# Performance work log

Measured on AMD Instinct MI355X. Metric: run time of the kernel, lower is better.

The kernel has to match this reference:

```python
import jax, jax.numpy as jnp
import numpy as np
import math

N = 30000; N0 = 18000; N1 = 12000; R = 5; E = 600000
H = 128; HM = 128; C = 8
L1 = 20.0; L2 = 30.0
THRESH = 0.3; THRESH_C = 1e-3
T_INNER = 20; K_OUTER = 8
EPS = 1e-5


def setup_inputs() -> dict:
    key = jax.random.key(0)
    ks = jax.random.split(key, 16)
    def w(k, shape):  # kaiming-ish fan_in init
        return jax.random.normal(k, shape, jnp.float32) / np.sqrt(shape[0])
    return {
        "feat0": jax.random.normal(ks[0], (N0, 256), jnp.float32),
        "feat1": jax.random.normal(ks[1], (N1, 128), jnp.float32),
        "W0": w(ks[2], (256, H)), "b0": jnp.zeros((H,), jnp.float32),
        "W1": w(ks[3], (128, H)), "b1": jnp.zeros((H,), jnp.float32),
        "Wm1": w(ks[4], (H, HM)), "bm1": jnp.zeros((HM,), jnp.float32),
        "Wm2": w(ks[5], (HM, HM)), "bm2": jnp.zeros((HM,), jnp.float32),
        "Wout": w(ks[6], (HM, C)), "bout": jnp.zeros((C,), jnp.float32),
        "src": jax.random.randint(ks[7], (E,), 0, N, jnp.int32),
        "dst": jax.random.randint(ks[8], (E,), 0, N, jnp.int32),
        "rel": jax.random.randint(ks[9], (E,), 0, R, jnp.int32),
    }


def _layernorm(z):
    m = z.mean(-1, keepdims=True)
    v = z.var(-1, keepdims=True)
    return (z - m) / jnp.sqrt(v + EPS)


def _forward(feat0, feat1, W0, b0, W1, b1, Wm1, bm1, Wm2, bm2, Wout, bout, src, dst, rel):
    # transfer (transf_type==2): per-type linear -> concat -> 2-layer MLP w/ layernorm
    h = jnp.concatenate([feat0 @ W0 + b0, feat1 @ W1 + b1], axis=0)   # (N, H)
    z = jax.nn.relu(_layernorm(h @ Wm1 + bm1))
    h = z @ Wm2 + bm2                                                 # (N, HM)
    # per-node standardization (torch std is unbiased, ddof=1), nan -> 0
    mu = h.mean(1, keepdims=True)
    sd = h.std(1, ddof=1, keepdims=True)
    out0 = jnp.nan_to_num((h - mu) / sd)

    # per-relation row degrees of the vertically stacked adjacency (R*N, N)
    key_e = rel * N + src                                             # (E,)
    deg = jax.ops.segment_sum(jnp.ones(E, jnp.float32), key_e, num_segments=R * N)
    safe = jnp.maximum(deg, 1.0)
    vals = jnp.where(deg > 0, 1.0 / safe, 0.0)[key_e]                 # row-normalized A weights
    dinv = jnp.where(deg > 0, 1.0 / jnp.sqrt(safe), 0.0)              # D^{-1/2}
    edge_dinv = dinv[key_e] * dinv[rel * N + dst]                     # (E,)
    active = (deg > 0).astype(jnp.float32).reshape(R, N)              # (R, N)

    def tv(x):  # relational total variation tr(X^T L_r X)/N, L_r = I - D^-1/2 A_r D^-1/2
        node_term = active @ (x * x).sum(1)                           # (R,)
        edot = (x[src] * x[dst]).sum(1)                               # (E,)
        edge_term = jax.ops.segment_sum(edge_dinv * edot, rel, num_segments=R)
        return (node_term - edge_term) / N

    ratio = 2.0 * L2 / L1
    c_l1tr = jnp.abs(tv(out0)).sum()
    u0 = jnp.full((R,), 1.0 / R, jnp.float32)

    def mirror_descent(u, w, l1tr):
        fi = l1tr + ratio
        def step(carry, t):
            u, act = carry
            T_t = jnp.sqrt(2.0 * math.log(R) / (t * fi * fi))
            u_ta = u * jnp.exp(-T_t * (ratio * u + w))
            u_new = u_ta / u_ta.sum()
            diff = jnp.sqrt(((u - u_new) ** 2).sum())
            u = jnp.where(act, u_new, u)
            return (u, act & (diff >= THRESH_C)), None
        ts = jnp.arange(1, T_INNER + 1, dtype=jnp.float32)
        (u, _), _ = jax.lax.scan(step, (u, jnp.array(True)), ts)
        return u

    def outer(carry, _):
        x, u, act = carry
        w = tv(x)
        l1tr = jnp.abs(w).sum()
        u = jnp.where(act, mirror_descent(u, w, l1tr), u)
        still = act & (l1tr / c_l1tr >= THRESH)
        ew = u[rel] * vals                                            # (E,)
        msg = jax.ops.segment_sum(ew[:, None] * x[dst], src, num_segments=N)  # (N, HM)
        x = jnp.where(still, x / (1.0 + L1) + (L1 / (1.0 + L1)) * msg, x)
        return (x, u, still), None

    (x, u, _), _ = jax.lax.scan(outer, (out0, u0, jnp.array(True)), None, length=K_OUTER)
    logits = x @ Wout + bout
    return logits, x, u


def reference(feat0, feat1, W0, b0, W1, b1, Wm1, bm1, Wm2, bm2, Wout, bout, src, dst, rel):
    return _forward(feat0, feat1, W0, b0, W1, b1, Wm1, bm1, Wm2, bm2, Wout, bout, src, dst, rel)
```

## Files before the change

### kernel.cpp

```cpp
#include <hip/hip_runtime.h>
#include <cmath>

typedef unsigned short ushort_t;
typedef unsigned int uint_t;

#define N_TOT 30000
#define N0_   18000
#define R_    5
#define E_    600000
#define RN    (R_ * N_TOT)
#define NC_   (N_TOT * 8)
#define NX_   (N_TOT * 128)
#define SCAN_NB ((RN + 1023) / 1024)

typedef __attribute__((ext_vector_type(8))) short bf16x8;
typedef __attribute__((ext_vector_type(4))) float f32x4;

__device__ __forceinline__ ushort_t f2bf(float f) {
    uint_t u = __float_as_uint(f);
    uint_t r = (u + 0x7fffu + ((u >> 16) & 1u)) >> 16;
    return (ushort_t)r;
}
__device__ __forceinline__ float bflo(uint_t v) { return __uint_as_float(v << 16); }
__device__ __forceinline__ float bfhi(uint_t v) { return __uint_as_float(v & 0xffff0000u); }

__global__ void init_kernel(float* ug, int* act) {
    if (threadIdx.x < 5) ug[threadIdx.x] = 0.2f;
    if (threadIdx.x == 0) act[0] = 1;
}

__global__ __launch_bounds__(256) void cvtfeat_kernel(const float* __restrict__ in,
                                                      ushort_t* __restrict__ out,
                                                      int nelem)
{
    int i = (blockIdx.x * 256 + threadIdx.x) * 4;
    if (i >= nelem) return;
    const float4 v = *(const float4*)(in + i);
    ushort_t o0 = f2bf(v.x), o1 = f2bf(v.y), o2 = f2bf(v.z), o3 = f2bf(v.w);
    uint_t p0 = (uint_t)o0 | ((uint_t)o1 << 16);
    uint_t p1 = (uint_t)o2 | ((uint_t)o3 << 16);
    uint2* op = (uint2*)(out + i);
    *op = make_uint2(p0, p1);
}

__global__ __launch_bounds__(256) void cvtw_kernel(const float* __restrict__ W,
                                                   ushort_t* __restrict__ wt, int K)
{
    int idx = blockIdx.x * 256 + threadIdx.x;
    if (idx >= 128 * K) return;
    int j = idx / K, k = idx - j * K;
    wt[idx] = f2bf(W[k * 128 + j]);
}

__global__ __launch_bounds__(256) void mlp_mfma_kernel(
    const ushort_t* __restrict__ fb0, const ushort_t* __restrict__ fb1,
    const ushort_t* __restrict__ wt0, const ushort_t* __restrict__ wt1,
    const ushort_t* __restrict__ wtm1, const ushort_t* __restrict__ wtm2,
    const float* __restrict__ b0, const float* __restrict__ b1,
    const float* __restrict__ bm1, const float* __restrict__ bm2,
    float* __restrict__ xout, ushort_t* __restrict__ xh)
{
    const int t = threadIdx.x;
    const int lane = t & 63;
    const int wv = t >> 6;
    const int lr = lane & 15;
    const int lg = lane >> 4;
    const int row0 = blockIdx.x * 32;

    __shared__ ushort_t hls[32][136];
    __shared__ float    tls[32][132];
    __shared__ ushort_t zls[32][136];

    #pragma unroll
    for (int mt = 0; mt < 2; ++mt) {
        const int rb = row0 + mt * 16;
        const bool is0 = (rb < N0_);
        const int r = min(rb + lr, N_TOT - 1);
        const ushort_t* __restrict__ fa =
            is0 ? fb0 + (size_t)r * 256 : fb1 + (size_t)(r - N0_) * 128;
        const ushort_t* __restrict__ wt = is0 ? wt0 : wt1;
        const int K = is0 ? 256 : 128;
        const int c0 = wv * 32 + lr;

        f32x4 a0 = {0.f, 0.f, 0.f, 0.f};
        f32x4 a1 = {0.f, 0.f, 0.f, 0.f};
        for (int ks = 0; ks < K; ks += 32) {
            const bf16x8 af = *(const bf16x8*)(fa + ks + lg * 8);
            const bf16x8 wb0 = *(const bf16x8*)(wt + (size_t)c0 * K + ks + lg * 8);
            const bf16x8 wb1 = *(const bf16x8*)(wt + (size_t)(c0 + 16) * K + ks + lg * 8);
            a0 = __builtin_amdgcn_mfma_f32_16x16x32_bf16(af, wb0, a0, 0, 0, 0);
            a1 = __builtin_amdgcn_mfma_f32_16x16x32_bf16(af, wb1, a1, 0, 0, 0);
        }
        const float bb0 = is0 ? b0[c0] : b1[c0];
        const float bb1 = is0 ? b0[c0 + 16] : b1[c0 + 16];
        #pragma unroll
        for (int j = 0; j < 4; ++j) {
            hls[mt * 16 + lg * 4 + j][c0]      = f2bf(a0[j] + bb0);
            hls[mt * 16 + lg * 4 + j][c0 + 16] = f2bf(a1[j] + bb1);
        }
    }
    __syncthreads();

    {
        const int c0 = wv * 32 + lr;
        f32x4 g00 = {0.f,0.f,0.f,0.f}, g01 = {0.f,0.f,0.f,0.f};
        f32x4 g10 = {0.f,0.f,0.f,0.f}, g11 = {0.f,0.f,0.f,0.f};
        for (int ks = 0; ks < 128; ks += 32) {
            const bf16x8 wb0 = *(const bf16x8*)(wtm1 + (size_t)c0 * 128 + ks + lg * 8);
            const bf16x8 wb1 = *(const bf16x8*)(wtm1 + (size_t)(c0 + 16) * 128 + ks + lg * 8);
            const bf16x8 af0 = *(const bf16x8*)(&hls[lr][ks + lg * 8]);
            const bf16x8 af1 = *(const bf16x8*)(&hls[16 + lr][ks + lg * 8]);
            g00 = __builtin_amdgcn_mfma_f32_16x16x32_bf16(af0, wb0, g00, 0, 0, 0);
            g01 = __builtin_amdgcn_mfma_f32_16x16x32_bf16(af0, wb1, g01, 0, 0, 0);
            g10 = __builtin_amdgcn_mfma_f32_16x16x32_bf16(af1, wb0, g10, 0, 0, 0);
            g11 = __builtin_amdgcn_mfma_f32_16x16x32_bf16(af1, wb1, g11, 0, 0, 0);
        }
        const float bb0 = bm1[c0], bb1 = bm1[c0 + 16];
        #pragma unroll
        for (int j = 0; j < 4; ++j) {
            tls[lg * 4 + j][c0]           = g00[j] + bb0;
            tls[lg * 4 + j][c0 + 16]      = g01[j] + bb1;
            tls[16 + lg * 4 + j][c0]      = g10[j] + bb0;
            tls[16 + lg * 4 + j][c0 + 16] = g11[j] + bb1;
        }
    }
    __syncthreads();

    {
        const int row = t >> 3, seg = t & 7;
        f32x4 v[4];
        float s = 0.f;
        #pragma unroll
        for (int i = 0; i < 4; ++i) {
            v[i] = *(const f32x4*)(&tls[row][seg * 16 + i * 4]);
            s += v[i][0] + v[i][1] + v[i][2] + v[i][3];
        }
        #pragma unroll
        for (int o = 1; o < 8; o <<= 1) s += __shfl_xor(s, o, 64);
        const float mean = s * (1.0f / 128.0f);
        float q = 0.f;
        #pragma unroll
        for (int i = 0; i < 4; ++i) {
            #pragma unroll
            for (int e = 0; e < 4; ++e) { float d = v[i][e] - mean; q = fmaf(d, d, q); }
        }
        #pragma unroll
        for (int o = 1; o < 8; o <<= 1) q += __shfl_xor(q, o, 64);
        const float inv = 1.0f / sqrtf(q * (1.0f / 128.0f) + 1e-5f);
        uint_t* zp = (uint_t*)&zls[row][0];
        #pragma unroll
        for (int i = 0; i < 4; ++i) {
            ushort_t z0 = f2bf(fmaxf((v[i][0] - mean) * inv, 0.0f));
            ushort_t z1 = f2bf(fmaxf((v[i][1] - mean) * inv, 0.0f));
            ushort_t z2 = f2bf(fmaxf((v[i][2] - mean) * inv, 0.0f));
            ushort_t z3 = f2bf(fmaxf((v[i][3] - mean) * inv, 0.0f));
            zp[(seg * 16 + i * 4) / 2]     = (uint_t)z0 | ((uint_t)z1 << 16);
            zp[(seg * 16 + i * 4) / 2 + 1] = (uint_t)z2 | ((uint_t)z3 << 16);
        }
    }
    __syncthreads();

    {
        const int c0 = wv * 32 + lr;
        f32x4 g00 = {0.f,0.f,0.f,0.f}, g01 = {0.f,0.f,0.f,0.f};
        f32x4 g10 = {0.f,0.f,0.f,0.f}, g11 = {0.f,0.f,0.f,0.f};
        for (int ks = 0; ks < 128; ks += 32) {
            const bf16x8 wb0 = *(const bf16x8*)(wtm2 + (size_t)c0 * 128 + ks + lg * 8);
            const bf16x8 wb1 = *(const bf16x8*)(wtm2 + (size_t)(c0 + 16) * 128 + ks + lg * 8);
            const bf16x8 af0 = *(const bf16x8*)(&zls[lr][ks + lg * 8]);
            const bf16x8 af1 = *(const bf16x8*)(&zls[16 + lr][ks + lg * 8]);
            g00 = __builtin_amdgcn_mfma_f32_16x16x32_bf16(af0, wb0, g00, 0, 0, 0);
            g01 = __builtin_amdgcn_mfma_f32_16x16x32_bf16(af0, wb1, g01, 0, 0, 0);
            g10 = __builtin_amdgcn_mfma_f32_16x16x32_bf16(af1, wb0, g10, 0, 0, 0);
            g11 = __builtin_amdgcn_mfma_f32_16x16x32_bf16(af1, wb1, g11, 0, 0, 0);
        }
        __syncthreads();
        const float bb0 = bm2[c0], bb1 = bm2[c0 + 16];
        #pragma unroll
        for (int j = 0; j < 4; ++j) {
            tls[lg * 4 + j][c0]           = g00[j] + bb0;
            tls[lg * 4 + j][c0 + 16]      = g01[j] + bb1;
            tls[16 + lg * 4 + j][c0]      = g10[j] + bb0;
            tls[16 + lg * 4 + j][c0 + 16] = g11[j] + bb1;
        }
    }
    __syncthreads();

    {
        const int row = t >> 3, seg = t & 7;
        const int n = row0 + row;
        f32x4 v[4];
        float s = 0.f;
        #pragma unroll
        for (int i = 0; i < 4; ++i) {
            v[i] = *(const f32x4*)(&tls[row][seg * 16 + i * 4]);
            s += v[i][0] + v[i][1] + v[i][2] + v[i][3];
        }
        #pragma unroll
        for (int o = 1; o < 8; o <<= 1) s += __shfl_xor(s, o, 64);
        const float mu = s * (1.0f / 128.0f);
        float q = 0.f;
        #pragma unroll
        for (int i = 0; i < 4; ++i) {
            #pragma unroll
            for (int e = 0; e < 4; ++e) { float d = v[i][e] - mu; q = fmaf(d, d, q); }
        }
        #pragma unroll
        for (int o = 1; o < 8; o <<= 1) q += __shfl_xor(q, o, 64);
        const float sd = sqrtf(q * (1.0f / 127.0f));
        const float inv = 1.0f / sd;
        if (n < N_TOT) {
            uint_t* xhp = (uint_t*)xh + (size_t)n * 64 + seg * 8;
            float* xop = xout + (size_t)n * 128 + seg * 16;
            #pragma unroll
            for (int i = 0; i < 4; ++i) {
                float rr[4];
                #pragma unroll
                for (int e = 0; e < 4; ++e) {
                    float r = (v[i][e] - mu) * inv;
                    if (!(fabsf(r) <= 3.402823466e38f)) {
                        r = (r != r) ? 0.0f : ((r > 0.0f) ? 3.402823466e38f : -3.402823466e38f);
                    }
                    rr[e] = r;
                }
                *(float4*)(xop + i * 4) = make_float4(rr[0], rr[1], rr[2], rr[3]);
                xhp[i * 2]     = (uint_t)f2bf(rr[0]) | ((uint_t)f2bf(rr[1]) << 16);
                xhp[i * 2 + 1] = (uint_t)f2bf(rr[2]) | ((uint_t)f2bf(rr[3]) << 16);
            }
        }
    }
}

__global__ void deg_kernel(const int* __restrict__ src, const int* __restrict__ rel,
                           int* __restrict__ deg_i)
{
    int e = blockIdx.x * 256 + threadIdx.x;
    if (e >= E_) return;
    atomicAdd(&deg_i[src[e] * R_ + rel[e]], 1);
}

__global__ void dinv_kernel(const int* __restrict__ deg_i, float* __restrict__ dinv)
{
    int i = blockIdx.x * 256 + threadIdx.x;
    if (i >= RN) return;
    int dg = deg_i[i];
    dinv[i] = (dg > 0) ? 1.0f / sqrtf((float)dg) : 0.0f;
}

__global__ __launch_bounds__(256) void scan1_kernel(const int* __restrict__ cnt,
                                                    int* __restrict__ rp,
                                                    int* __restrict__ bsum)
{
    __shared__ int wsum[4];
    const int t = threadIdx.x, lane = t & 63, w = t >> 6;
    const int i0 = blockIdx.x * 1024 + t * 4;
    const int v0 = (i0 + 0 < RN) ? cnt[i0 + 0] : 0;
    const int v1 = (i0 + 1 < RN) ? cnt[i0 + 1] : 0;
    const int v2 = (i0 + 2 < RN) ? cnt[i0 + 2] : 0;
    const int v3 = (i0 + 3 < RN) ? cnt[i0 + 3] : 0;
    const int s = v0 + v1 + v2 + v3;
    int sc = s;
    #pragma unroll
    for (int o = 1; o < 64; o <<= 1) { int tmp = __shfl_up(sc, o, 64); if (lane >= o) sc += tmp; }
    if (lane == 63) wsum[w] = sc;
    __syncthreads();
    int woff = 0;
    #pragma unroll
    for (int i = 0; i < 3; ++i) if (i < w) woff += wsum[i];
    int run = woff + sc - s;
    if (i0 + 0 < RN) rp[i0 + 0] = run; run += v0;
    if (i0 + 1 < RN) rp[i0 + 1] = run; run += v1;
    if (i0 + 2 < RN) rp[i0 + 2] = run; run += v2;
    if (i0 + 3 < RN) rp[i0 + 3] = run;
    if (t == 255) bsum[blockIdx.x] = woff + sc;
}

__global__ __launch_bounds__(256) void scan2_kernel(const int* __restrict__ bsum,
                                                    int* __restrict__ boff,
                                                    int* __restrict__ rp)
{
    __shared__ int wsum[4];
    const int t = threadIdx.x, lane = t & 63, w = t >> 6;
    const int v = (t < SCAN_NB) ? bsum[t] : 0;
    int sc = v;
    #pragma unroll
    for (int o = 1; o < 64; o <<= 1) { int tmp = __shfl_up(sc, o, 64); if (lane >= o) sc += tmp; }
    if (lane == 63) wsum[w] = sc;
    __syncthreads();
    int woff = 0;
    #pragma unroll
    for (int i = 0; i < 3; ++i) if (i < w) woff += wsum[i];
    boff[t] = woff + sc - v;
    if (t == 0) rp[RN] = E_;
}

__global__ __launch_bounds__(256) void scan3_kernel(int* __restrict__ rp,
                                                    const int* __restrict__ boff)
{
    const int off = boff[blockIdx.x];
    if (off == 0) return;
    const int i0 = blockIdx.x * 1024 + threadIdx.x * 4;
    if (i0 + 3 < RN) {
        int4* p = (int4*)(rp + i0);
        int4 q = *p;
        q.x += off; q.y += off; q.z += off; q.w += off;
        *p = q;
    } else {
        for (int i = 0; i < 4; ++i)
            if (i0 + i < RN) rp[i0 + i] += off;
    }
}

__global__ void scatter_kernel(const int* __restrict__ src, const int* __restrict__ dst,
                               const int* __restrict__ rel, const int* __restrict__ rp,
                               int* __restrict__ fill, const int* __restrict__ deg_i,
                               const float* __restrict__ dinv,
                               int* __restrict__ csr_dst, float* __restrict__ csr_w,
                               float* __restrict__ csr_edinv)
{
    int e = blockIdx.x * 256 + threadIdx.x;
    if (e >= E_) return;
    int s = src[e], r = rel[e], d = dst[e];
    int key = s * R_ + r;
    int pos = rp[key] + atomicAdd(&fill[key], 1);
    csr_dst[pos] = d;
    csr_w[pos] = 1.0f / (float)deg_i[key];
    csr_edinv[pos] = dinv[key] * dinv[d * R_ + r];
}

__global__ __launch_bounds__(256) void tv_kernel(
    const ushort_t* __restrict__ xh, const int* __restrict__ rp,
    const int* __restrict__ csr_dst, const float* __restrict__ csr_edinv,
    const int* __restrict__ act, int k, float* __restrict__ accbuf)
{
    if (act[k] == 0) return;
    const int lane = threadIdx.x & 63;
    const int wv = threadIdx.x >> 6;
    const int wid = blockIdx.x * 4 + wv;
    const int nw = gridDim.x * 4;
    float na[5] = {0, 0, 0, 0, 0};
    float ea[5] = {0, 0, 0, 0, 0};
    for (int n = wid; n < N_TOT; n += nw) {
        const int b0 = __builtin_amdgcn_readfirstlane(rp[n * R_ + 0]);
        const int b1 = __builtin_amdgcn_readfirstlane(rp[n * R_ + 1]);
        const int b2 = __builtin_amdgcn_readfirstlane(rp[n * R_ + 2]);
        const int b3 = __builtin_amdgcn_readfirstlane(rp[n * R_ + 3]);
        const int b4 = __builtin_amdgcn_readfirstlane(rp[n * R_ + 4]);
        const int b5 = __builtin_amdgcn_readfirstlane(rp[n * R_ + 5]);
        const uint_t vs = ((const uint_t*)(xh + (size_t)n * 128))[lane];
        const float sx = bflo(vs), sy = bfhi(vs);
        const float pp = fmaf(sx, sx, sy * sy);
        if (b1 > b0) na[0] += pp;
        if (b2 > b1) na[1] += pp;
        if (b3 > b2) na[2] += pp;
        if (b4 > b3) na[3] += pp;
        if (b5 > b4) na[4] += pp;
        int e = b0;
        for (; e + 4 <= b5; e += 4) {
            const int dn0 = csr_dst[e + 0];
            const int dn1 = csr_dst[e + 1];
            const int dn2 = csr_dst[e + 2];
            const int dn3 = csr_dst[e + 3];
            const float w0 = csr_edinv[e + 0];
            const float w1 = csr_edinv[e + 1];
            const float w2 = csr_edinv[e + 2];
            const float w3 = csr_edinv[e + 3];
            const uint_t v0 = ((const uint_t*)(xh + (size_t)dn0 * 128))[lane];
            const uint_t v1 = ((const uint_t*)(xh + (size_t)dn1 * 128))[lane];
            const uint_t v2 = ((const uint_t*)(xh + (size_t)dn2 * 128))[lane];
            const uint_t v3 = ((const uint_t*)(xh + (size_t)dn3 * 128))[lane];
            const float d0 = w0 * fmaf(sx, bflo(v0), sy * bfhi(v0));
            const float d1 = w1 * fmaf(sx, bflo(v1), sy * bfhi(v1));
            const float d2 = w2 * fmaf(sx, bflo(v2), sy * bfhi(v2));
            const float d3 = w3 * fmaf(sx, bflo(v3), sy * bfhi(v3));
            const int r0 = (e + 0 >= b1) + (e + 0 >= b2) + (e + 0 >= b3) + (e + 0 >= b4);
            const int r1 = (e + 1 >= b1) + (e + 1 >= b2) + (e + 1 >= b3) + (e + 1 >= b4);
            const int r2 = (e + 2 >= b1) + (e + 2 >= b2) + (e + 2 >= b3) + (e + 2 >= b4);
            const int r3 = (e + 3 >= b1) + (e + 3 >= b2) + (e + 3 >= b3) + (e + 3 >= b4);
            #pragma unroll
            for (int rr = 0; rr < 5; ++rr) {
                ea[rr] += (r0 == rr ? d0 : 0.0f) + (r1 == rr ? d1 : 0.0f) +
                          (r2 == rr ? d2 : 0.0f) + (r3 == rr ? d3 : 0.0f);
            }
        }
        for (; e < b5; ++e) {
            const int dn0 = csr_dst[e];
            const float w0 = csr_edinv[e];
            const uint_t v0 = ((const uint_t*)(xh + (size_t)dn0 * 128))[lane];
            const float d0 = w0 * fmaf(sx, bflo(v0), sy * bfhi(v0));
            const int r0 = (e >= b1) + (e >= b2) + (e >= b3) + (e >= b4);
            #pragma unroll
            for (int rr = 0; rr < 5; ++rr)
                ea[rr] += (r0 == rr ? d0 : 0.0f);
        }
    }
    __shared__ float sacc[4][10];
    #pragma unroll
    for (int r = 0; r < 5; ++r) {
        float a = na[r], b = ea[r];
        for (int o = 32; o > 0; o >>= 1) {
            a += __shfl_down(a, o, 64);
            b += __shfl_down(b, o, 64);
        }
        if (lane == 0) { sacc[wv][r] = a; sacc[wv][5 + r] = b; }
    }
    __syncthreads();
    if (threadIdx.x < 10) {
        float t = sacc[0][threadIdx.x] + sacc[1][threadIdx.x] +
                  sacc[2][threadIdx.x] + sacc[3][threadIdx.x];
        atomicAdd(&accbuf[k * 16 + threadIdx.x], t);
    }
}

__global__ void scalar_kernel(const float* __restrict__ accbuf, float* __restrict__ ug,
                              float* __restrict__ c_l1, int* __restrict__ act, int k)
{
    if (blockIdx.x != 0 || threadIdx.x >= 8) return;
    const int r = threadIdx.x;
    const int a = act[k];
    float w = (r < 5) ? (accbuf[k * 16 + r] - accbuf[k * 16 + 5 + r]) * (1.0f / 30000.0f)
                      : 0.0f;
    float l1 = fabsf(w);
    for (int o = 4; o > 0; o >>= 1) l1 += __shfl_xor(l1, o, 8);
    if (k == 0 && r == 0) c_l1[0] = l1;
    if (!a) { if (r == 0) act[k + 1] = 0; return; }
    float u = (r < 5) ? ug[r] : 0.0f;
    const float fi = l1 + 3.0f;
    bool mact = true;
    for (int t = 1; t <= 20; ++t) {
        float T = sqrtf(3.2188758248682006f / ((float)t * fi * fi));
        float ta = u * expf(-T * (3.0f * u + w));
        float ssum = ta;
        for (int o = 4; o > 0; o >>= 1) ssum += __shfl_xor(ssum, o, 8);
        float un = ta / ssum;
        float d0 = u - un;
        float dq = d0 * d0;
        for (int o = 4; o > 0; o >>= 1) dq += __shfl_xor(dq, o, 8);
        if (mact) u = un;
        mact = mact && (sqrtf(dq) >= 1e-3f);
    }
    if (r < 5) ug[r] = u;
    if (r == 0) act[k + 1] = (l1 / c_l1[0] >= 0.3f) ? 1 : 0;
}

__global__ __launch_bounds__(256) void msg_upd_kernel(
    float* __restrict__ x, const ushort_t* __restrict__ xh_in,
    ushort_t* __restrict__ xh_out,
    const int* __restrict__ rp, const int* __restrict__ csr_dst,
    const float* __restrict__ csr_w, const float* __restrict__ ug,
    const int* __restrict__ act, int k)
{
    if (act[k + 1] == 0) return;
    const int lane = threadIdx.x & 63;
    const int wid = blockIdx.x * 4 + (threadIdx.x >> 6);
    const int nw = gridDim.x * 4;
    const float u0 = ug[0], u1 = ug[1], u2 = ug[2], u3 = ug[3], u4 = ug[4];
    for (int n = wid; n < N_TOT; n += nw) {
        const int b1 = __builtin_amdgcn_readfirstlane(rp[n * R_ + 1]);
        const int b2 = __builtin_amdgcn_readfirstlane(rp[n * R_ + 2]);
        const int b3 = __builtin_amdgcn_readfirstlane(rp[n * R_ + 3]);
        const int b4 = __builtin_amdgcn_readfirstlane(rp[n * R_ + 4]);
        const int b0 = __builtin_amdgcn_readfirstlane(rp[n * R_ + 0]);
        const int b5 = __builtin_amdgcn_readfirstlane(rp[n * R_ + 5]);
        float ax0 = 0.0f, ay0 = 0.0f, ax1 = 0.0f, ay1 = 0.0f;
        int e = b0;
        for (; e + 4 <= b5; e += 4) {
            const int r0 = (e + 0 >= b1) + (e + 0 >= b2) + (e + 0 >= b3) + (e + 0 >= b4);
            const int r1 = (e + 1 >= b1) + (e + 1 >= b2) + (e + 1 >= b3) + (e + 1 >= b4);
            const int r2 = (e + 2 >= b1) + (e + 2 >= b2) + (e + 2 >= b3) + (e + 2 >= b4);
            const int r3 = (e + 3 >= b1) + (e + 3 >= b2) + (e + 3 >= b3) + (e + 3 >= b4);
            const float uu0 = (r0 == 0) ? u0 : (r0 == 1) ? u1 : (r0 == 2) ? u2 : (r0 == 3) ? u3 : u4;
            const float uu1 = (r1 == 0) ? u0 : (r1 == 1) ? u1 : (r1 == 2) ? u2 : (r1 == 3) ? u3 : u4;
            const float uu2 = (r2 == 0) ? u0 : (r2 == 1) ? u1 : (r2 == 2) ? u2 : (r2 == 3) ? u3 : u4;
            const float uu3 = (r3 == 0) ? u0 : (r3 == 1) ? u1 : (r3 == 2) ? u2 : (r3 == 3) ? u3 : u4;
            const int dn0 = csr_dst[e + 0];
            const int dn1 = csr_dst[e + 1];
            const int dn2 = csr_dst[e + 2];
            const int dn3 = csr_dst[e + 3];
            const float w0 = uu0 * csr_w[e + 0];
            const float w1 = uu1 * csr_w[e + 1];
            const float w2 = uu2 * csr_w[e + 2];
            const float w3 = uu3 * csr_w[e + 3];
            const uint_t v0 = ((const uint_t*)(xh_in + (size_t)dn0 * 128))[lane];
            const uint_t v1 = ((const uint_t*)(xh_in + (size_t)dn1 * 128))[lane];
            const uint_t v2 = ((const uint_t*)(xh_in + (size_t)dn2 * 128))[lane];
            const uint_t v3 = ((const uint_t*)(xh_in + (size_t)dn3 * 128))[lane];
            ax0 = fmaf(w0, bflo(v0), ax0); ay0 = fmaf(w0, bfhi(v0), ay0);
            ax1 = fmaf(w1, bflo(v1), ax1); ay1 = fmaf(w1, bfhi(v1), ay1);
            ax0 = fmaf(w2, bflo(v2), ax0); ay0 = fmaf(w2, bfhi(v2), ay0);
            ax1 = fmaf(w3, bflo(v3), ax1); ay1 = fmaf(w3, bfhi(v3), ay1);
        }
        for (; e < b5; ++e) {
            const int r0 = (e >= b1) + (e >= b2) + (e >= b3) + (e >= b4);
            const float uu0 = (r0 == 0) ? u0 : (r0 == 1) ? u1 : (r0 == 2) ? u2 : (r0 == 3) ? u3 : u4;
            const int dn0 = csr_dst[e];
            const float w0 = uu0 * csr_w[e];
            const uint_t v0 = ((const uint_t*)(xh_in + (size_t)dn0 * 128))[lane];
            ax0 = fmaf(w0, bflo(v0), ax0);
            ay0 = fmaf(w0, bfhi(v0), ay0);
        }
        const float ci = 1.0f / 21.0f, cb = 20.0f / 21.0f;
        float2* xp = (float2*)(x + (size_t)n * 128);
        const float2 xs = xp[lane];
        const float nx_ = fmaf(cb, ax0 + ax1, xs.x * ci);
        const float ny_ = fmaf(cb, ay0 + ay1, xs.y * ci);
        xp[lane] = make_float2(nx_, ny_);
        ((uint_t*)(xh_out + (size_t)n * 128))[lane] =
            ((uint_t)f2bf(ny_) << 16) | (uint_t)f2bf(nx_);
    }
}

__global__ __launch_bounds__(256) void final_kernel(const float* __restrict__ x,
                                                    const float* __restrict__ Wout,
                                                    const float* __restrict__ bout,
                                                    const float* __restrict__ ug,
                                                    float* __restrict__ out)
{
    const int nl = threadIdx.x >> 7;
    const int n = blockIdx.x * 2 + nl;
    const int j = threadIdx.x & 127;
    const int lane = threadIdx.x & 63;
    const int wv = threadIdx.x >> 6;
    float xv = x[(size_t)n * 128 + j];
    out[(size_t)NC_ + (size_t)n * 128 + j] = xv;
    float p[8];
    #pragma unroll
    for (int c = 0; c < 8; ++c) p[c] = xv * Wout[j * 8 + c];
    #pragma unroll
    for (int c = 0; c < 8; ++c)
        for (int o = 32; o > 0; o >>= 1) p[c] += __shfl_down(p[c], o, 64);
    __shared__ float sp[4][8];
    if (lane == 0) {
        #pragma unroll
        for (int c = 0; c < 8; ++c) sp[wv][c] = p[c];
    }
    __syncthreads();
    if (j < 8) {
        int c = j;
        out[(size_t)n * 8 + c] = bout[c] + sp[2 * nl][c] + sp[2 * nl + 1][c];
    }
    if (blockIdx.x == 0 && threadIdx.x < 5)
        out[(size_t)NC_ + (size_t)NX_ + threadIdx.x] = ug[threadIdx.x];
}

extern "C" void kernel_launch(void* const* d_in, const int* in_sizes, int n_in,
                              void* d_out, int out_size, void* d_ws, size_t ws_size,
                              hipStream_t stream)
{
    const float* feat0 = (const float*)d_in[0];
    const float* feat1 = (const float*)d_in[1];
    const float* W0   = (const float*)d_in[2];
    const float* b0   = (const float*)d_in[3];
    const float* W1   = (const float*)d_in[4];
    const float* b1   = (const float*)d_in[5];
    const float* Wm1  = (const float*)d_in[6];
    const float* bm1  = (const float*)d_in[7];
    const float* Wm2  = (const float*)d_in[8];
    const float* bm2  = (const float*)d_in[9];
    const float* Wout = (const float*)d_in[10];
    const float* bout = (const float*)d_in[11];
    const int* src = (const int*)d_in[12];
    const int* dst = (const int*)d_in[13];
    const int* rel = (const int*)d_in[14];
    float* out = (float*)d_out;

    char* p = (char*)d_ws;
    auto alloc = [&](size_t bytes) { char* q = p; p += (bytes + 255) & ~(size_t)255; return q; };
    float*    xbuf      = (float*)   alloc((size_t)NX_ * 4);
    ushort_t* xh0       = (ushort_t*)alloc((size_t)NX_ * 2);
    ushort_t* xh1       = (ushort_t*)alloc((size_t)NX_ * 2);
    ushort_t* fb0       = (ushort_t*)alloc((size_t)N0_ * 256 * 2);
    ushort_t* fb1       = (ushort_t*)alloc((size_t)(N_TOT - N0_) * 128 * 2);
    ushort_t* wt0       = (ushort_t*)alloc((size_t)128 * 256 * 2);
    ushort_t* wt1       = (ushort_t*)alloc((size_t)128 * 128 * 2);
    ushort_t* wtm1      = (ushort_t*)alloc((size_t)128 * 128 * 2);
    ushort_t* wtm2      = (ushort_t*)alloc((size_t)128 * 128 * 2);
    int*      deg_i     = (int*)     alloc((size_t)RN * 4);
    float*    dinv      = (float*)   alloc((size_t)RN * 4);
    int*      rp        = (int*)     alloc(((size_t)RN + 1) * 4);
    int*      fill      = (int*)     alloc((size_t)RN * 4);
    int*      bsum      = (int*)     alloc((size_t)SCAN_NB * 4);
    int*      boff      = (int*)     alloc(256 * 4);
    int*      csr_dst   = (int*)     alloc((size_t)E_ * 4);
    float*    csr_w     = (float*)   alloc((size_t)E_ * 4);
    float*    csr_edinv = (float*)   alloc((size_t)E_ * 4);
    float*    accbuf    = (float*)   alloc(128 * 4);
    float*    ug        = (float*)   alloc(64);
    float*    c_l1      = (float*)   alloc(64);
    int*      act       = (int*)     alloc(64);

    hipMemsetAsync(deg_i, 0, (size_t)RN * 4, stream);
    hipMemsetAsync(fill, 0, (size_t)RN * 4, stream);
    hipMemsetAsync(accbuf, 0, 128 * 4, stream);
    init_kernel<<<1, 64, 0, stream>>>(ug, act);

    cvtfeat_kernel<<<(N0_ * 256 / 4 + 255) / 256, 256, 0, stream>>>(feat0, fb0, N0_ * 256);
    cvtfeat_kernel<<<((N_TOT - N0_) * 128 / 4 + 255) / 256, 256, 0, stream>>>(
        feat1, fb1, (N_TOT - N0_) * 128);
    cvtw_kernel<<<(128 * 256 + 255) / 256, 256, 0, stream>>>(W0, wt0, 256);
    cvtw_kernel<<<(128 * 128 + 255) / 256, 256, 0, stream>>>(W1, wt1, 128);
    cvtw_kernel<<<(128 * 128 + 255) / 256, 256, 0, stream>>>(Wm1, wtm1, 128);
    cvtw_kernel<<<(128 * 128 + 255) / 256, 256, 0, stream>>>(Wm2, wtm2, 128);

    mlp_mfma_kernel<<<(N_TOT + 31) / 32, 256, 0, stream>>>(
        fb0, fb1, wt0, wt1, wtm1, wtm2, b0, b1, bm1, bm2, xbuf, xh0);

    deg_kernel<<<(E_ + 255) / 256, 256, 0, stream>>>(src, rel, deg_i);
    dinv_kernel<<<(RN + 255) / 256, 256, 0, stream>>>(deg_i, dinv);
    scan1_kernel<<<SCAN_NB, 256, 0, stream>>>(deg_i, rp, bsum);
    scan2_kernel<<<1, 256, 0, stream>>>(bsum, boff, rp);
    scan3_kernel<<<SCAN_NB, 256, 0, stream>>>(rp, boff);
    scatter_kernel<<<(E_ + 255) / 256, 256, 0, stream>>>(src, dst, rel, rp, fill,
                                                         deg_i, dinv,
                                                         csr_dst, csr_w, csr_edinv);

    ushort_t* ha = xh0;
    ushort_t* hb = xh1;
    for (int k = 0; k < 8; ++k) {
        tv_kernel<<<2048, 256, 0, stream>>>(ha, rp, csr_dst, csr_edinv, act, k, accbuf);
        scalar_kernel<<<1, 64, 0, stream>>>(accbuf, ug, c_l1, act, k);
        msg_upd_kernel<<<2048, 256, 0, stream>>>(xbuf, ha, hb, rp, csr_dst, csr_w,
                                                 ug, act, k);
        ushort_t* t = ha; ha = hb; hb = t;
    }

    final_kernel<<<N_TOT / 2, 256, 0, stream>>>(xbuf, Wout, bout, ug, out);
}
```

Before: 445.2 us.

## Fuse TV and message gathers into one pass with per-relation partial messages

The tv kernel now also accumulates per-relation weighted neighbour sums and stores them as fp16 in a 5xN buffer. A lightweight elementwise apply kernel then combines them with the relation weights u once they are known. This removes the second irregular gather over all edges in each outer iteration. CSR fields are packed into one int4 per edge so each edge needs a single vector load. The cost is extra register pressure for the 10 accumulators, a 5x per-node fp16 write and read, and fp16 rounding of the partial messages.

```diff
diff --git a/kernel.cpp b/kernel.cpp
--- a/kernel.cpp
+++ b/kernel.cpp
@@ -1,4 +1,5 @@
 #include <hip/hip_runtime.h>
+#include <hip/hip_fp16.h>
 #include <cmath>
 
 typedef unsigned short ushort_t;
@@ -11,6 +12,7 @@
 #define RN    (R_ * N_TOT)
 #define NC_   (N_TOT * 8)
 #define NX_   (N_TOT * 128)
+#define NL_   (N_TOT * 64)
 #define SCAN_NB ((RN + 1023) / 1024)
 
 typedef __attribute__((ext_vector_type(8))) short bf16x8;
@@ -315,23 +317,23 @@
                                const int* __restrict__ rel, const int* __restrict__ rp,
                                int* __restrict__ fill, const int* __restrict__ deg_i,
                                const float* __restrict__ dinv,
-                               int* __restrict__ csr_dst, float* __restrict__ csr_w,
-                               float* __restrict__ csr_edinv)
+                               int4* __restrict__ csr_pk)
 {
     int e = blockIdx.x * 256 + threadIdx.x;
     if (e >= E_) return;
     int s = src[e], r = rel[e], d = dst[e];
     int key = s * R_ + r;
     int pos = rp[key] + atomicAdd(&fill[key], 1);
-    csr_dst[pos] = d;
-    csr_w[pos] = 1.0f / (float)deg_i[key];
-    csr_edinv[pos] = dinv[key] * dinv[d * R_ + r];
-}
-
-__global__ __launch_bounds__(256) void tv_kernel(
+    float edinv = dinv[key] * dinv[d * R_ + r];
+    float w = 1.0f / (float)deg_i[key];
+    csr_pk[pos] = make_int4(d, __float_as_int(edinv), __float_as_int(w), 0);
+}
+
+__global__ __launch_bounds__(256) void gather_kernel(
     const ushort_t* __restrict__ xh, const int* __restrict__ rp,
-    const int* __restrict__ csr_dst, const float* __restrict__ csr_edinv,
-    const int* __restrict__ act, int k, float* __restrict__ accbuf)
+    const int4* __restrict__ csr_pk,
+    const int* __restrict__ act, int k, float* __restrict__ accbuf,
+    uint_t* __restrict__ mbuf)
 {
     if (act[k] == 0) return;
     const int lane = threadIdx.x & 63;
@@ -355,24 +357,26 @@
         if (b3 > b2) na[2] += pp;
         if (b4 > b3) na[3] += pp;
         if (b5 > b4) na[4] += pp;
+        float mx[5] = {0, 0, 0, 0, 0};
+        float my[5] = {0, 0, 0, 0, 0};
         int e = b0;
         for (; e + 4 <= b5; e += 4) {
-            const int dn0 = csr_dst[e + 0];
-            const int dn1 = csr_dst[e + 1];
-            const int dn2 = csr_dst[e + 2];
-            const int dn3 = csr_dst[e + 3];
-            const float w0 = csr_edinv[e + 0];
-            const float w1 = csr_edinv[e + 1];
-            const float w2 = csr_edinv[e + 2];
-            const float w3 = csr_edinv[e + 3];
-            const uint_t v0 = ((const uint_t*)(xh + (size_t)dn0 * 128))[lane];
-            const uint_t v1 = ((const uint_t*)(xh + (size_t)dn1 * 128))[lane];
-            const uint_t v2 = ((const uint_t*)(xh + (size_t)dn2 * 128))[lane];
-            const uint_t v3 = ((const uint_t*)(xh + (size_t)dn3 * 128))[lane];
-            const float d0 = w0 * fmaf(sx, bflo(v0), sy * bfhi(v0));
-            const float d1 = w1 * fmaf(sx, bflo(v1), sy * bfhi(v1));
-            const float d2 = w2 * fmaf(sx, bflo(v2), sy * bfhi(v2));
-            const float d3 = w3 * fmaf(sx, bflo(v3), sy * bfhi(v3));
+            int4 p0 = csr_pk[e + 0];
+            int4 p1 = csr_pk[e + 1];
+            int4 p2 = csr_pk[e + 2];
+            int4 p3 = csr_pk[e + 3];
+            const uint_t v0 = ((const uint_t*)(xh + (size_t)p0.x * 128))[lane];
+            const uint_t v1 = ((const uint_t*)(xh + (size_t)p1.x * 128))[lane];
+            const uint_t v2 = ((const uint_t*)(xh + (size_t)p2.x * 128))[lane];
+            const uint_t v3 = ((const uint_t*)(xh + (size_t)p3.x * 128))[lane];
+            const float x0 = bflo(v0), y0 = bfhi(v0);
+            const float x1 = bflo(v1), y1 = bfhi(v1);
+            const float x2 = bflo(v2), y2 = bfhi(v2);
+            const float x3 = bflo(v3), y3 = bfhi(v3);
+            const float d0 = __int_as_float(p0.y) * fmaf(sx, x0, sy * y0);
+            const float d1 = __int_as_float(p1.y) * fmaf(sx, x1, sy * y1);
+            const float d2 = __int_as_float(p2.y) * fmaf(sx, x2, sy * y2);
+            const float d3 = __int_as_float(p3.y) * fmaf(sx, x3, sy * y3);
             const int r0 = (e + 0 >= b1) + (e + 0 >= b2) + (e + 0 >= b3) + (e + 0 >= b4);
             const int r1 = (e + 1 >= b1) + (e + 1 >= b2) + (e + 1 >= b3) + (e + 1 >= b4);
             const int r2 = (e + 2 >= b1) + (e + 2 >= b2) + (e + 2 >= b3) + (e + 2 >= b4);
@@ -381,17 +385,33 @@
             for (int rr = 0; rr < 5; ++rr) {
                 ea[rr] += (r0 == rr ? d0 : 0.0f) + (r1 == rr ? d1 : 0.0f) +
                           (r2 == rr ? d2 : 0.0f) + (r3 == rr ? d3 : 0.0f);
+                const float ws0 = (r0 == rr) ? __int_as_float(p0.z) : 0.0f;
+                const float ws1 = (r1 == rr) ? __int_as_float(p1.z) : 0.0f;
+                const float ws2 = (r2 == rr) ? __int_as_float(p2.z) : 0.0f;
+                const float ws3 = (r3 == rr) ? __int_as_float(p3.z) : 0.0f;
+                mx[rr] = fmaf(ws0, x0, fmaf(ws1, x1, fmaf(ws2, x2, fmaf(ws3, x3, mx[rr]))));
+                my[rr] = fmaf(ws0, y0, fmaf(ws1, y1, fmaf(ws2, y2, fmaf(ws3, y3, my[rr]))));
             }
         }
         for (; e < b5; ++e) {
-            const int dn0 = csr_dst[e];
-            const float w0 = csr_edinv[e];
-            const uint_t v0 = ((const uint_t*)(xh + (size_t)dn0 * 128))[lane];
-            const float d0 = w0 * fmaf(sx, bflo(v0), sy * bfhi(v0));
+            int4 p0 = csr_pk[e];
+            const uint_t v0 = ((const uint_t*)(xh + (size_t)p0.x * 128))[lane];
+            const float x0 = bflo(v0), y0 = bfhi(v0);
+            const float d0 = __int_as_float(p0.y) * fmaf(sx, x0, sy * y0);
             const int r0 = (e >= b1) + (e >= b2) + (e >= b3) + (e >= b4);
             #pragma unroll
-            for (int rr = 0; rr < 5; ++rr)
+            for (int rr = 0; rr < 5; ++rr) {
                 ea[rr] += (r0 == rr ? d0 : 0.0f);
+                const float ws0 = (r0 == rr) ? __int_as_float(p0.z) : 0.0f;
+                mx[rr] = fmaf(ws0, x0, mx[rr]);
+                my[rr] = fmaf(ws0, y0, my[rr]);
+            }
+        }
+        #pragma unroll
+        for (int rr = 0; rr < 5; ++rr) {
+            __half2 hm = __floats2half2_rn(mx[rr], my[rr]);
+            mbuf[(size_t)rr * NL_ + (size_t)n * 64 + lane] =
+                *reinterpret_cast<const uint_t*>(&hm);
         }
     }
     __shared__ float sacc[4][10];
@@ -443,71 +463,37 @@
     if (r == 0) act[k + 1] = (l1 / c_l1[0] >= 0.3f) ? 1 : 0;
 }
 
-__global__ __launch_bounds__(256) void msg_upd_kernel(
-    float* __restrict__ x, const ushort_t* __restrict__ xh_in,
-    ushort_t* __restrict__ xh_out,
-    const int* __restrict__ rp, const int* __restrict__ csr_dst,
-    const float* __restrict__ csr_w, const float* __restrict__ ug,
+__global__ __launch_bounds__(256) void apply_kernel(
+    float* __restrict__ x, ushort_t* __restrict__ xh_out,
+    const uint_t* __restrict__ mbuf, const float* __restrict__ ug,
     const int* __restrict__ act, int k)
 {
     if (act[k + 1] == 0) return;
-    const int lane = threadIdx.x & 63;
-    const int wid = blockIdx.x * 4 + (threadIdx.x >> 6);
-    const int nw = gridDim.x * 4;
+    const int tid = blockIdx.x * 256 + threadIdx.x;
+    if (tid >= NL_) return;
     const float u0 = ug[0], u1 = ug[1], u2 = ug[2], u3 = ug[3], u4 = ug[4];
-    for (int n = wid; n < N_TOT; n += nw) {
-        const int b1 = __builtin_amdgcn_readfirstlane(rp[n * R_ + 1]);
-        const int b2 = __builtin_amdgcn_readfirstlane(rp[n * R_ + 2]);
-        const int b3 = __builtin_amdgcn_readfirstlane(rp[n * R_ + 3]);
-        const int b4 = __builtin_amdgcn_readfirstlane(rp[n * R_ + 4]);
-        const int b0 = __builtin_amdgcn_readfirstlane(rp[n * R_ + 0]);
-        const int b5 = __builtin_amdgcn_readfirstlane(rp[n * R_ + 5]);
-        float ax0 = 0.0f, ay0 = 0.0f, ax1 = 0.0f, ay1 = 0.0f;
-        int e = b0;
-        for (; e + 4 <= b5; e += 4) {
-            const int r0 = (e + 0 >= b1) + (e + 0 >= b2) + (e + 0 >= b3) + (e + 0 >= b4);
-            const int r1 = (e + 1 >= b1) + (e + 1 >= b2) + (e + 1 >= b3) + (e + 1 >= b4);
-            const int r2 = (e + 2 >= b1) + (e + 2 >= b2) + (e + 2 >= b3) + (e + 2 >= b4);
-            const int r3 = (e + 3 >= b1) + (e + 3 >= b2) + (e + 3 >= b3) + (e + 3 >= b4);
-            const float uu0 = (r0 == 0) ? u0 : (r0 == 1) ? u1 : (r0 == 2) ? u2 : (r0 == 3) ? u3 : u4;
-            const float uu1 = (r1 == 0) ? u0 : (r1 == 1) ? u1 : (r1 == 2) ? u2 : (r1 == 3) ? u3 : u4;
-            const float uu2 = (r2 == 0) ? u0 : (r2 == 1) ? u1 : (r2 == 2) ? u2 : (r2 == 3) ? u3 : u4;
-            const float uu3 = (r3 == 0) ? u0 : (r3 == 1) ? u1 : (r3 == 2) ? u2 : (r3 == 3) ? u3 : u4;
-            const int dn0 = csr_dst[e + 0];
-            const int dn1 = csr_dst[e + 1];
-            const int dn2 = csr_dst[e + 2];
-            const int dn3 = csr_dst[e + 3];
-            const float w0 = uu0 * csr_w[e + 0];
-            const float w1 = uu1 * csr_w[e + 1];
-            const float w2 = uu2 * csr_w[e + 2];
-            const float w3 = uu3 * csr_w[e + 3];
-            const uint_t v0 = ((const uint_t*)(xh_in + (size_t)dn0 * 128))[lane];
-            const uint_t v1 = ((const uint_t*)(xh_in + (size_t)dn1 * 128))[lane];
-            const uint_t v2 = ((const uint_t*)(xh_in + (size_t)dn2 * 128))[lane];
-            const uint_t v3 = ((const uint_t*)(xh_in + (size_t)dn3 * 128))[lane];
-            ax0 = fmaf(w0, bflo(v0), ax0); ay0 = fmaf(w0, bfhi(v0), ay0);
-            ax1 = fmaf(w1, bflo(v1), ax1); ay1 = fmaf(w1, bfhi(v1), ay1);
-            ax0 = fmaf(w2, bflo(v2), ax0); ay0 = fmaf(w2, bfhi(v2), ay0);
-            ax1 = fmaf(w3, bflo(v3), ax1); ay1 = fmaf(w3, bfhi(v3), ay1);
-        }
-        for (; e < b5; ++e) {
-            const int r0 = (e >= b1) + (e >= b2) + (e >= b3) + (e >= b4);
-            const float uu0 = (r0 == 0) ? u0 : (r0 == 1) ? u1 : (r0 == 2) ? u2 : (r0 == 3) ? u3 : u4;
-            const int dn0 = csr_dst[e];
-            const float w0 = uu0 * csr_w[e];
-            const uint_t v0 = ((const uint_t*)(xh_in + (size_t)dn0 * 128))[lane];
-            ax0 = fmaf(w0, bflo(v0), ax0);
-            ay0 = fmaf(w0, bfhi(v0), ay0);
-        }
-        const float ci = 1.0f / 21.0f, cb = 20.0f / 21.0f;
-        float2* xp = (float2*)(x + (size_t)n * 128);
-        const float2 xs = xp[lane];
-        const float nx_ = fmaf(cb, ax0 + ax1, xs.x * ci);
-        const float ny_ = fmaf(cb, ay0 + ay1, xs.y * ci);
-        xp[lane] = make_float2(nx_, ny_);
-        ((uint_t*)(xh_out + (size_t)n * 128))[lane] =
-            ((uint_t)f2bf(ny_) << 16) | (uint_t)f2bf(nx_);
-    }
+
+    uint_t w0 = mbuf[(size_t)0 * NL_ + tid];
+    uint_t w1 = mbuf[(size_t)1 * NL_ + tid];
+    uint_t w2 = mbuf[(size_t)2 * NL_ + tid];
+    uint_t w3 = mbuf[(size_t)3 * NL_ + tid];
+    uint_t w4 = mbuf[(size_t)4 * NL_ + tid];
+    const float2 m0 = __half22float2(*reinterpret_cast<const __half2*>(&w0));
+    const float2 m1 = __half22float2(*reinterpret_cast<const __half2*>(&w1));
+    const float2 m2 = __half22float2(*reinterpret_cast<const __half2*>(&w2));
+    const float2 m3 = __half22float2(*reinterpret_cast<const __half2*>(&w3));
+    const float2 m4 = __half22float2(*reinterpret_cast<const __half2*>(&w4));
+
+    const float sm_x = u0 * m0.x + u1 * m1.x + u2 * m2.x + u3 * m3.x + u4 * m4.x;
+    const float sm_y = u0 * m0.y + u1 * m1.y + u2 * m2.y + u3 * m3.y + u4 * m4.y;
+
+    const float ci = 1.0f / 21.0f, cb = 20.0f / 21.0f;
+    float2* xp = (float2*)x;
+    const float2 xs = xp[tid];
+    const float nx_ = fmaf(cb, sm_x, xs.x * ci);
+    const float ny_ = fmaf(cb, sm_y, xs.y * ci);
+    xp[tid] = make_float2(nx_, ny_);
+    ((uint_t*)xh_out)[tid] = ((uint_t)f2bf(ny_) << 16) | (uint_t)f2bf(nx_);
 }
 
 __global__ __launch_bounds__(256) void final_kernel(const float* __restrict__ x,
@@ -569,6 +555,7 @@
     float*    xbuf      = (float*)   alloc((size_t)NX_ * 4);
     ushort_t* xh0       = (ushort_t*)alloc((size_t)NX_ * 2);
     ushort_t* xh1       = (ushort_t*)alloc((size_t)NX_ * 2);
+    uint_t*   mbuf      = (uint_t*)  alloc((size_t)R_ * NL_ * 4);
     ushort_t* fb0       = (ushort_t*)alloc((size_t)N0_ * 256 * 2);
     ushort_t* fb1       = (ushort_t*)alloc((size_t)(N_TOT - N0_) * 128 * 2);
     ushort_t* wt0       = (ushort_t*)alloc((size_t)128 * 256 * 2);
@@ -581,9 +568,7 @@
     int*      fill      = (int*)     alloc((size_t)RN * 4);
     int*      bsum      = (int*)     alloc((size_t)SCAN_NB * 4);
     int*      boff      = (int*)     alloc(256 * 4);
-    int*      csr_dst   = (int*)     alloc((size_t)E_ * 4);
-    float*    csr_w     = (float*)   alloc((size_t)E_ * 4);
-    float*    csr_edinv = (float*)   alloc((size_t)E_ * 4);
+    int4*     csr_pk    = (int4*)    alloc((size_t)E_ * 16);
     float*    accbuf    = (float*)   alloc(128 * 4);
     float*    ug        = (float*)   alloc(64);
     float*    c_l1      = (float*)   alloc(64);
@@ -611,16 +596,14 @@
     scan2_kernel<<<1, 256, 0, stream>>>(bsum, boff, rp);
     scan3_kernel<<<SCAN_NB, 256, 0, stream>>>(rp, boff);
     scatter_kernel<<<(E_ + 255) / 256, 256, 0, stream>>>(src, dst, rel, rp, fill,
-                                                         deg_i, dinv,
-                                                         csr_dst, csr_w, csr_edinv);
+                                                         deg_i, dinv, csr_pk);
 
     ushort_t* ha = xh0;
     ushort_t* hb = xh1;
     for (int k = 0; k < 8; ++k) {
-        tv_kernel<<<2048, 256, 0, stream>>>(ha, rp, csr_dst, csr_edinv, act, k, accbuf);
+        gather_kernel<<<2048, 256, 0, stream>>>(ha, rp, csr_pk, act, k, accbuf, mbuf);
         scalar_kernel<<<1, 64, 0, stream>>>(accbuf, ug, c_l1, act, k);
-        msg_upd_kernel<<<2048, 256, 0, stream>>>(xbuf, ha, hb, rp, csr_dst, csr_w,
-                                                 ug, act, k);
+        apply_kernel<<<(NL_ + 255) / 256, 256, 0, stream>>>(xbuf, hb, mbuf, ug, act, k);
         ushort_t* t = ha; ha = hb; hb = t;
     }
 
```

After: 434.0 us. 2.5% less time.
